# Performance work log

Measured on AMD Instinct MI355X. Metric: run time of the kernel, lower is better.

## Reference

```python
import jax, jax.numpy as jnp
import numpy as np

B = 262144
N = 256      # mode size of every TT core
R = 8        # tt_rank
D = 8        # number of cores = 7 state dims + 1 action dim
STD = 0.001


def setup_inputs() -> dict:
    key = jax.random.key(0)
    ks = jax.random.split(key, D + 2)
    inp = {}
    # TT cores: G0 (1,N,R), G1..G6 (R,N,R), G7 (R,N,1)
    inp["G0"] = jax.random.normal(ks[0], (1, N, R), dtype=jnp.float32) * STD
    for k in range(1, D - 1):
        inp[f"G{k}"] = jax.random.normal(ks[k], (R, N, R), dtype=jnp.float32) * STD
    inp[f"G{D-1}"] = jax.random.normal(ks[D - 1], (R, N, 1), dtype=jnp.float32) * STD
    inp["states"] = jax.random.randint(ks[D], (B, 7), 0, N, dtype=jnp.int32)
    inp["actions"] = jax.random.randint(ks[D + 1], (B,), 0, N, dtype=jnp.int32)
    return inp


def reference(G0, G1, G2, G3, G4, G5, G6, G7, states, actions):
    # mode 'q_sa': concat state indices with action index -> (B, D)
    idx = jnp.concatenate(
        [states.reshape(-1, 7), actions.reshape(-1, 1)], axis=1
    )
    cores = [G0, G1, G2, G3, G4, G5, G6, G7]
    # t3f.gather_nd: chain of per-core gathers + tiny batched matmuls.
    # vec starts as the gathered slice of the first core: (B, R)
    vec = cores[0][0, idx[:, 0], :]
    for k in range(1, D):
        # gather slices along mode axis: (B, r_prev, r_next)
        sl = jnp.transpose(jnp.take(cores[k], idx[:, k], axis=1), (1, 0, 2))
        vec = jnp.einsum("br,brs->bs", vec, sl)
    # final vec has shape (B, 1); Q(s,a) values per batch element
    return vec[:, 0]
```

## Files before the change

### kernel.cpp

```cpp
#include <hip/hip_runtime.h>


#define NN 256
#define RR 8
#define NR 2048
#define U67_OFF 524288
#define GT_OFF  1048576

__device__ __forceinline__ unsigned short f2bf_rne(float f) {
    unsigned int u = __float_as_uint(f);
    u += 0x7FFFu + ((u >> 16) & 1u);
    return (unsigned short)(u >> 16);
}

__device__ __forceinline__ uint4 pack8bf(const float* a) {
    return make_uint4(
        f2bf_rne(a[0]) | ((unsigned int)f2bf_rne(a[1]) << 16),
        f2bf_rne(a[2]) | ((unsigned int)f2bf_rne(a[3]) << 16),
        f2bf_rne(a[4]) | ((unsigned int)f2bf_rne(a[5]) << 16),
        f2bf_rne(a[6]) | ((unsigned int)f2bf_rne(a[7]) << 16));
}

__global__ __launch_bounds__(256) void build_tables(
    const float* __restrict__ G0, const float* __restrict__ G1,
    const float* __restrict__ G2, const float* __restrict__ G3,
    const float* __restrict__ G4, const float* __restrict__ G5,
    const float* __restrict__ G6, const float* __restrict__ G7,
    unsigned short* __restrict__ wsb) {
    const int t = threadIdx.x;
    const int bid = blockIdx.x;

    if (bid < NN) {
        const int n0 = bid, n1 = t;
        float acc[RR] = {0.f,0.f,0.f,0.f,0.f,0.f,0.f,0.f};
#pragma unroll
        for (int r = 0; r < RR; ++r) {
            float ar = G0[n0 * RR + r];
            const float4* p = (const float4*)(G1 + r * NR + n1 * RR);
            float4 x = p[0], y = p[1];
            acc[0] += ar * x.x; acc[1] += ar * x.y;
            acc[2] += ar * x.z; acc[3] += ar * x.w;
            acc[4] += ar * y.x; acc[5] += ar * y.y;
            acc[6] += ar * y.z; acc[7] += ar * y.w;
        }
        *(uint4*)(wsb + n0 * 2048 + n1 * 8) = pack8bf(acc);
    } else if (bid < 2 * NN) {
        const int n6 = bid - NN, n7 = t;
        float g7v[RR];
#pragma unroll
        for (int s = 0; s < RR; ++s) g7v[s] = G7[s * NN + n7];
        float u[RR];
#pragma unroll
        for (int r = 0; r < RR; ++r) {
            float acc = 0.f;
#pragma unroll
            for (int s = 0; s < RR; ++s)
                acc += G6[r * NR + n6 * RR + s] * g7v[s];
            u[r] = acc;
        }
        *(uint4*)(wsb + U67_OFF + n6 * 2048 + n7 * 8) = pack8bf(u);
    } else {
        const int q = bid - 2 * NN;
        const int k = q >> 3;
        const int chunk = q & 7;
        const float* __restrict__ Gk =
            (k == 0) ? G2 : (k == 1) ? G3 : (k == 2) ? G4 : G5;
        const int n = chunk * 32 + (t >> 3);
        const int r = t & 7;
        const float4* src = (const float4*)(Gk + r * NR + n * RR);
        float4 x = src[0], y = src[1];
        float a[8] = {x.x, x.y, x.z, x.w, y.x, y.y, y.z, y.w};
        *(uint4*)(wsb + GT_OFF + k * 16384 + n * 64 + r * 8) = pack8bf(a);
    }
}

#define BF2F_LO(u) __uint_as_float((u) << 16)
#define BF2F_HI(u) __uint_as_float((u) & 0xFFFF0000u)

#define BSTAGE(koff, nidx)                                                  \
    do {                                                                    \
        const uint4* mp =                                                   \
            (const uint4*)(wsb + GT_OFF + (koff)*16384 + (nidx)*64);        \
        float nv0 = 0.f, nv1 = 0.f, nv2 = 0.f, nv3 = 0.f;                   \
        float nv4 = 0.f, nv5 = 0.f, nv6 = 0.f, nv7 = 0.f;                   \
        _Pragma("unroll") for (int r = 0; r < 8; ++r) {                     \
            uint4 u = mp[r];                                                \
            float vr = v[r];                                                \
            nv0 += vr * BF2F_LO(u.x); nv1 += vr * BF2F_HI(u.x);             \
            nv2 += vr * BF2F_LO(u.y); nv3 += vr * BF2F_HI(u.y);             \
            nv4 += vr * BF2F_LO(u.z); nv5 += vr * BF2F_HI(u.z);             \
            nv6 += vr * BF2F_LO(u.w); nv7 += vr * BF2F_HI(u.w);             \
        }                                                                   \
        v[0] = nv0; v[1] = nv1; v[2] = nv2; v[3] = nv3;                     \
        v[4] = nv4; v[5] = nv5; v[6] = nv6; v[7] = nv7;                     \
    } while (0)

__global__ __launch_bounds__(256) void tt_gather(
    const unsigned short* __restrict__ wsb,
    const int* __restrict__ states, const int* __restrict__ actions,
    float* __restrict__ out, int B) {
    __shared__ int ibuf[NN * 7];

    const int t = threadIdx.x;
    const int b = blockIdx.x * 256 + t;

    {
        const int* gsrc = states + (size_t)blockIdx.x * 256 * 7;
        const int lim = B * 7 - blockIdx.x * 256 * 7;
#pragma unroll
        for (int k = 0; k < 7; ++k) {
            int j = t + (k << 8);
            if (j < lim) ibuf[j] = gsrc[j];
        }
    }
    __syncthreads();

    const bool active = (b < B);
    const int* row = ibuf + t * 7;
    const int s0 = row[0] & 255;
    const int s1 = row[1] & 255;
    const int s2 = row[2] & 255;
    const int s3 = row[3] & 255;
    const int s4 = row[4] & 255;
    const int s5 = row[5] & 255;
    const int s6 = row[6] & 255;
    const int a7 = actions[active ? b : 0] & 255;

    float v[8];
    {
        uint4 u = *(const uint4*)(wsb + s0 * 2048 + s1 * 8);
        v[0] = BF2F_LO(u.x); v[1] = BF2F_HI(u.x);
        v[2] = BF2F_LO(u.y); v[3] = BF2F_HI(u.y);
        v[4] = BF2F_LO(u.z); v[5] = BF2F_HI(u.z);
        v[6] = BF2F_LO(u.w); v[7] = BF2F_HI(u.w);
    }

    BSTAGE(0, s2);
    BSTAGE(1, s3);
    BSTAGE(2, s4);
    BSTAGE(3, s5);

    float q;
    {
        uint4 u = *(const uint4*)(wsb + U67_OFF + s6 * 2048 + a7 * 8);
        q = v[0] * BF2F_LO(u.x) + v[1] * BF2F_HI(u.x)
          + v[2] * BF2F_LO(u.y) + v[3] * BF2F_HI(u.y)
          + v[4] * BF2F_LO(u.z) + v[5] * BF2F_HI(u.z)
          + v[6] * BF2F_LO(u.w) + v[7] * BF2F_HI(u.w);
    }
    if (active) out[b] = q;
}

extern "C" void kernel_launch(void* const* d_in, const int* in_sizes, int n_in,
                              void* d_out, int out_size, void* d_ws, size_t ws_size,
                              hipStream_t stream) {
    const float* G0 = (const float*)d_in[0];
    const float* G1 = (const float*)d_in[1];
    const float* G2 = (const float*)d_in[2];
    const float* G3 = (const float*)d_in[3];
    const float* G4 = (const float*)d_in[4];
    const float* G5 = (const float*)d_in[5];
    const float* G6 = (const float*)d_in[6];
    const float* G7 = (const float*)d_in[7];
    const int* states  = (const int*)d_in[8];
    const int* actions = (const int*)d_in[9];
    float* out = (float*)d_out;
    int B = in_sizes[9];

    unsigned short* wsb = (unsigned short*)d_ws;

    hipLaunchKernelGGL(build_tables, dim3(2 * NN + 32), dim3(256), 0, stream,
                       G0, G1, G2, G3, G4, G5, G6, G7, wsb);

    hipLaunchKernelGGL(tt_gather, dim3((B + 255) / 256), dim3(256), 0, stream,
                       wsb, states, actions, out, B);
}
```

Before: 101.5 us.

## Precontract G2·G3 and G4·G5 into pair tables and issue all gathers upfront

Adds per-call precomputed 8x8 product tables for core pairs (G2,G3) and (G4,G5), indexed by both mode indices, so the gather kernel does two mat-vecs instead of four. All table loads are issued together before any arithmetic, so the random gathers can overlap. The cost is a larger build step (65536 8x8 products per pair) and 8 MB of bf16 tables that are far less cache-friendly than the old small per-core tables. Products are rounded to bf16 once per pair rather than per core.

After: 104.9 us. 3.4% more time.

```diff
diff --git a/kernel.cpp b/kernel.cpp
--- a/kernel.cpp
+++ b/kernel.cpp
@@ -5,7 +5,8 @@
 #define RR 8
 #define NR 2048
 #define U67_OFF 524288
-#define GT_OFF  1048576
+#define M23_OFF 1048576
+#define M45_OFF 5242880
 
 __device__ __forceinline__ unsigned short f2bf_rne(float f) {
     unsigned int u = __float_as_uint(f);
@@ -60,37 +61,86 @@
         }
         *(uint4*)(wsb + U67_OFF + n6 * 2048 + n7 * 8) = pack8bf(u);
     } else {
-        const int q = bid - 2 * NN;
-        const int k = q >> 3;
-        const int chunk = q & 7;
-        const float* __restrict__ Gk =
-            (k == 0) ? G2 : (k == 1) ? G3 : (k == 2) ? G4 : G5;
-        const int n = chunk * 32 + (t >> 3);
-        const int r = t & 7;
-        const float4* src = (const float4*)(Gk + r * NR + n * RR);
-        float4 x = src[0], y = src[1];
-        float a[8] = {x.x, x.y, x.z, x.w, y.x, y.y, y.z, y.w};
-        *(uint4*)(wsb + GT_OFF + k * 16384 + n * 64 + r * 8) = pack8bf(a);
+        const bool is23 = (bid < 3 * NN);
+        const int sa = bid - (is23 ? 2 * NN : 3 * NN);
+        const int sb = t;
+        const float* __restrict__ A = is23 ? G2 : G4;
+        const float* __restrict__ Bc = is23 ? G3 : G5;
+        const size_t base =
+            (is23 ? M23_OFF : M45_OFF) + ((size_t)sa * NN + sb) * 64;
+
+        float bmat[RR][RR];
+#pragma unroll
+        for (int m = 0; m < RR; ++m) {
+            const float4* p = (const float4*)(Bc + m * NR + sb * RR);
+            float4 x = p[0], y = p[1];
+            bmat[m][0] = x.x; bmat[m][1] = x.y;
+            bmat[m][2] = x.z; bmat[m][3] = x.w;
+            bmat[m][4] = y.x; bmat[m][5] = y.y;
+            bmat[m][6] = y.z; bmat[m][7] = y.w;
+        }
+#pragma unroll
+        for (int r = 0; r < RR; ++r) {
+            float c[RR] = {0.f,0.f,0.f,0.f,0.f,0.f,0.f,0.f};
+#pragma unroll
+            for (int m = 0; m < RR; ++m) {
+                float a = A[r * NR + sa * RR + m];
+#pragma unroll
+                for (int s = 0; s < RR; ++s) c[s] += a * bmat[m][s];
+            }
+            *(uint4*)(wsb + base + r * 8) = pack8bf(c);
+        }
     }
 }
 
 #define BF2F_LO(u) __uint_as_float((u) << 16)
 #define BF2F_HI(u) __uint_as_float((u) & 0xFFFF0000u)
 
-#define BSTAGE(koff, nidx)                                                  \
+#define MATVEC(m0,m1,m2,m3,m4,m5,m6,m7)                                     \
     do {                                                                    \
-        const uint4* mp =                                                   \
-            (const uint4*)(wsb + GT_OFF + (koff)*16384 + (nidx)*64);        \
         float nv0 = 0.f, nv1 = 0.f, nv2 = 0.f, nv3 = 0.f;                   \
         float nv4 = 0.f, nv5 = 0.f, nv6 = 0.f, nv7 = 0.f;                   \
-        _Pragma("unroll") for (int r = 0; r < 8; ++r) {                     \
-            uint4 u = mp[r];                                                \
-            float vr = v[r];                                                \
-            nv0 += vr * BF2F_LO(u.x); nv1 += vr * BF2F_HI(u.x);             \
-            nv2 += vr * BF2F_LO(u.y); nv3 += vr * BF2F_HI(u.y);             \
-            nv4 += vr * BF2F_LO(u.z); nv5 += vr * BF2F_HI(u.z);             \
-            nv6 += vr * BF2F_LO(u.w); nv7 += vr * BF2F_HI(u.w);             \
-        }                                                                   \
+        uint4 mr;                                                           \
+        mr = m0; { float vr = v[0];                                         \
+            nv0 += vr * BF2F_LO(mr.x); nv1 += vr * BF2F_HI(mr.x);           \
+            nv2 += vr * BF2F_LO(mr.y); nv3 += vr * BF2F_HI(mr.y);           \
+            nv4 += vr * BF2F_LO(mr.z); nv5 += vr * BF2F_HI(mr.z);           \
+            nv6 += vr * BF2F_LO(mr.w); nv7 += vr * BF2F_HI(mr.w); }         \
+        mr = m1; { float vr = v[1];                                         \
+            nv0 += vr * BF2F_LO(mr.x); nv1 += vr * BF2F_HI(mr.x);           \
+            nv2 += vr * BF2F_LO(mr.y); nv3 += vr * BF2F_HI(mr.y);           \
+            nv4 += vr * BF2F_LO(mr.z); nv5 += vr * BF2F_HI(mr.z);           \
+            nv6 += vr * BF2F_LO(mr.w); nv7 += vr * BF2F_HI(mr.w); }         \
+        mr = m2; { float vr = v[2];                                         \
+            nv0 += vr * BF2F_LO(mr.x); nv1 += vr * BF2F_HI(mr.x);           \
+            nv2 += vr * BF2F_LO(mr.y); nv3 += vr * BF2F_HI(mr.y);           \
+            nv4 += vr * BF2F_LO(mr.z); nv5 += vr * BF2F_HI(mr.z);           \
+            nv6 += vr * BF2F_LO(mr.w); nv7 += vr * BF2F_HI(mr.w); }         \
+        mr = m3; { float vr = v[3];                                         \
+            nv0 += vr * BF2F_LO(mr.x); nv1 += vr * BF2F_HI(mr.x);           \
+            nv2 += vr * BF2F_LO(mr.y); nv3 += vr * BF2F_HI(mr.y);           \
+            nv4 += vr * BF2F_LO(mr.z); nv5 += vr * BF2F_HI(mr.z);           \
+            nv6 += vr * BF2F_LO(mr.w); nv7 += vr * BF2F_HI(mr.w); }         \
+        mr = m4; { float vr = v[4];                                         \
+            nv0 += vr * BF2F_LO(mr.x); nv1 += vr * BF2F_HI(mr.x);           \
+            nv2 += vr * BF2F_LO(mr.y); nv3 += vr * BF2F_HI(mr.y);           \
+            nv4 += vr * BF2F_LO(mr.z); nv5 += vr * BF2F_HI(mr.z);           \
+            nv6 += vr * BF2F_LO(mr.w); nv7 += vr * BF2F_HI(mr.w); }         \
+        mr = m5; { float vr = v[5];                                         \
+            nv0 += vr * BF2F_LO(mr.x); nv1 += vr * BF2F_HI(mr.x);           \
+            nv2 += vr * BF2F_LO(mr.y); nv3 += vr * BF2F_HI(mr.y);           \
+            nv4 += vr * BF2F_LO(mr.z); nv5 += vr * BF2F_HI(mr.z);           \
+            nv6 += vr * BF2F_LO(mr.w); nv7 += vr * BF2F_HI(mr.w); }         \
+        mr = m6; { float vr = v[6];                                         \
+            nv0 += vr * BF2F_LO(mr.x); nv1 += vr * BF2F_HI(mr.x);           \
+            nv2 += vr * BF2F_LO(mr.y); nv3 += vr * BF2F_HI(mr.y);           \
+            nv4 += vr * BF2F_LO(mr.z); nv5 += vr * BF2F_HI(mr.z);           \
+            nv6 += vr * BF2F_LO(mr.w); nv7 += vr * BF2F_HI(mr.w); }         \
+        mr = m7; { float vr = v[7];                                         \
+            nv0 += vr * BF2F_LO(mr.x); nv1 += vr * BF2F_HI(mr.x);           \
+            nv2 += vr * BF2F_LO(mr.y); nv3 += vr * BF2F_HI(mr.y);           \
+            nv4 += vr * BF2F_LO(mr.z); nv5 += vr * BF2F_HI(mr.z);           \
+            nv6 += vr * BF2F_LO(mr.w); nv7 += vr * BF2F_HI(mr.w); }         \
         v[0] = nv0; v[1] = nv1; v[2] = nv2; v[3] = nv3;                     \
         v[4] = nv4; v[5] = nv5; v[6] = nv6; v[7] = nv7;                     \
     } while (0)
@@ -126,28 +176,31 @@
     const int s6 = row[6] & 255;
     const int a7 = actions[active ? b : 0] & 255;
 
+    const uint4* pv = (const uint4*)(wsb + ((size_t)s0 * NN + s1) * 8);
+    const uint4* pa = (const uint4*)(wsb + M23_OFF + ((size_t)s2 * NN + s3) * 64);
+    const uint4* pb = (const uint4*)(wsb + M45_OFF + ((size_t)s4 * NN + s5) * 64);
+    const uint4* pu = (const uint4*)(wsb + U67_OFF + ((size_t)s6 * NN + a7) * 8);
+
+    uint4 uv = pv[0];
+    uint4 a0 = pa[0], a1 = pa[1], a2 = pa[2], a3 = pa[3];
+    uint4 a4 = pa[4], a5 = pa[5], a6 = pa[6], a7q = pa[7];
+    uint4 b0 = pb[0], b1 = pb[1], b2 = pb[2], b3 = pb[3];
+    uint4 b4 = pb[4], b5 = pb[5], b6 = pb[6], b7 = pb[7];
+    uint4 uu = pu[0];
+
     float v[8];
-    {
-        uint4 u = *(const uint4*)(wsb + s0 * 2048 + s1 * 8);
-        v[0] = BF2F_LO(u.x); v[1] = BF2F_HI(u.x);
-        v[2] = BF2F_LO(u.y); v[3] = BF2F_HI(u.y);
-        v[4] = BF2F_LO(u.z); v[5] = BF2F_HI(u.z);
-        v[6] = BF2F_LO(u.w); v[7] = BF2F_HI(u.w);
-    }
-
-    BSTAGE(0, s2);
-    BSTAGE(1, s3);
-    BSTAGE(2, s4);
-    BSTAGE(3, s5);
-
-    float q;
-    {
-        uint4 u = *(const uint4*)(wsb + U67_OFF + s6 * 2048 + a7 * 8);
-        q = v[0] * BF2F_LO(u.x) + v[1] * BF2F_HI(u.x)
-          + v[2] * BF2F_LO(u.y) + v[3] * BF2F_HI(u.y)
-          + v[4] * BF2F_LO(u.z) + v[5] * BF2F_HI(u.z)
-          + v[6] * BF2F_LO(u.w) + v[7] * BF2F_HI(u.w);
-    }
+    v[0] = BF2F_LO(uv.x); v[1] = BF2F_HI(uv.x);
+    v[2] = BF2F_LO(uv.y); v[3] = BF2F_HI(uv.y);
+    v[4] = BF2F_LO(uv.z); v[5] = BF2F_HI(uv.z);
+    v[6] = BF2F_LO(uv.w); v[7] = BF2F_HI(uv.w);
+
+    MATVEC(a0, a1, a2, a3, a4, a5, a6, a7q);
+    MATVEC(b0, b1, b2, b3, b4, b5, b6, b7);
+
+    float q = v[0] * BF2F_LO(uu.x) + v[1] * BF2F_HI(uu.x)
+            + v[2] * BF2F_LO(uu.y) + v[3] * BF2F_HI(uu.y)
+            + v[4] * BF2F_LO(uu.z) + v[5] * BF2F_HI(uu.z)
+            + v[6] * BF2F_LO(uu.w) + v[7] * BF2F_HI(uu.w);
     if (active) out[b] = q;
 }
 
@@ -169,7 +222,7 @@
 
     unsigned short* wsb = (unsigned short*)d_ws;
 
-    hipLaunchKernelGGL(build_tables, dim3(2 * NN + 32), dim3(256), 0, stream,
+    hipLaunchKernelGGL(build_tables, dim3(4 * NN), dim3(256), 0, stream,
                        G0, G1, G2, G3, G4, G5, G6, G7, wsb);
 
     hipLaunchKernelGGL(tt_gather, dim3((B + 255) / 256), dim3(256), 0, stream,
```
